# Kernel optimization log

Measured on AMD Instinct MI355X. Metric: run time of the kernel, lower is better.

The kernel has to match this reference:

```python
import jax, jax.numpy as jnp
import numpy as np

B, L, D, H, S, E, FF = 4, 2048, 1024, 16, 512, 8, 4096
DH = D // H  # head dim = 64
EPS = 1e-5


def setup_inputs() -> dict:
    key = jax.random.key(0)
    ks = jax.random.split(key, 12)
    std = 0.02
    return {
        "x": jax.random.normal(ks[0], (B, L, D), jnp.float32),
        "slot_query": jax.random.normal(ks[1], (H, S, DH), jnp.float32) * std,
        "slot_key": jax.random.normal(ks[2], (H, S, DH), jnp.float32) * std,
        "w_dispatch_k": jax.random.normal(ks[3], (D, D), jnp.float32) * std,
        "w_dispatch_v": jax.random.normal(ks[4], (D, D), jnp.float32) * std,
        "w_combine_q": jax.random.normal(ks[5], (D, D), jnp.float32) * std,
        "w_in": jax.random.normal(ks[6], (E, FF, D), jnp.float32) * std,
        "b_in": jnp.zeros((E, FF), jnp.float32),
        "w_out": jax.random.normal(ks[7], (E, D, FF), jnp.float32) * std,
        "b_out": jnp.zeros((E, D), jnp.float32),
        "pre_norm_w": jnp.ones((D,), jnp.float32),
        "pre_norm_b": jnp.zeros((D,), jnp.float32),
    }


def _layer_norm(x, w, b, eps=EPS):
    m = jnp.mean(x, axis=-1, keepdims=True)
    v = jnp.mean(jnp.square(x - m), axis=-1, keepdims=True)
    return (x - m) * jax.lax.rsqrt(v + eps) * w + b


def _sdpa(q, k, v):
    # q: (..., Q, d), k: (..., K, d), v: (..., K, d)
    scale = 1.0 / np.sqrt(q.shape[-1])
    scores = jnp.einsum("...qd,...kd->...qk", q, k) * scale
    p = jax.nn.softmax(scores, axis=-1)
    return jnp.einsum("...qk,...kd->...qd", p, v)


def _split_heads(t):  # (B, N, D) -> (B, H, N, DH)
    b, n, _ = t.shape
    return t.reshape(b, n, H, DH).transpose(0, 2, 1, 3)


def _merge_heads(t):  # (B, H, N, DH) -> (B, N, D)
    b, h, n, d = t.shape
    return t.transpose(0, 2, 1, 3).reshape(b, n, h * d)


def reference(x, slot_query, slot_key, w_dispatch_k, w_dispatch_v, w_combine_q,
              w_in, b_in, w_out, b_out, pre_norm_w, pre_norm_b):
    # pre-norm
    xn = _layer_norm(x, pre_norm_w, pre_norm_b)

    # ---- dispatch: slots attend to tokens ----
    k = _split_heads(xn @ w_dispatch_k.T)        # (B,H,L,DH)
    v = _split_heads(xn @ w_dispatch_v.T)        # (B,H,L,DH)
    y = _sdpa(slot_query[None], k, v)            # (B,H,S,DH)
    y = _merge_heads(y)                          # (B,S,D)

    # ---- experts: batched per-expert MLP with relu^2 activation ----
    y = y.reshape(B, E, S // E, D)
    h = jnp.einsum("besd,efd->besf", y, w_in) + b_in[None, :, None, :]
    h = jnp.square(jax.nn.relu(h))               # relu2
    eo = jnp.einsum("besf,edf->besd", h, w_out) + b_out[None, :, None, :]
    eo = eo.reshape(B, S, D)

    # ---- combine: tokens attend to slots ----
    q = _split_heads(xn @ w_combine_q.T)         # (B,H,L,DH)
    vc = _split_heads(eo)                        # (B,H,S,DH)
    o = _sdpa(q, slot_key[None], vc)             # (B,H,L,DH)
    return _merge_heads(o)                       # (B,L,D)
```

## Files before the change

### kernel.cpp

```cpp
#include <hip/hip_runtime.h>
#include <hip/hip_bf16.h>

#define B_  4
#define L_  2048
#define D_  1024
#define H_  16
#define S_  512
#define E_  8
#define FF_ 4096
#define DH_ 64

typedef _Float16 half8 __attribute__((ext_vector_type(8)));
typedef _Float16 half4v __attribute__((ext_vector_type(4)));
typedef float floatx4 __attribute__((ext_vector_type(4)));
typedef unsigned short u16;

__device__ inline u16 f2h(float v) {
  _Float16 x = (_Float16)v;
  return __builtin_bit_cast(u16, x);
}

__device__ inline void gload_lds16(const void* g, void* l) {
  __builtin_amdgcn_global_load_lds(
      (const __attribute__((address_space(1))) void*)g,
      (__attribute__((address_space(3))) void*)l, 16, 0, 0);
}

__device__ inline int swz(int row, int colh) {
  return row * 64 + (colh ^ ((row & 7) << 3));
}
__device__ inline int swz1(int row, int colh) {
  return row * 64 + ((colh & ~7) ^ ((row & 7) << 3)) + (colh & 7);
}

__global__ __launch_bounds__(256) void ln_f16(const float* __restrict__ x,
    const float* __restrict__ w, const float* __restrict__ bb,
    u16* __restrict__ xn) {
  int row = blockIdx.x;
  int tid = threadIdx.x;
  float4 v = ((const float4*)(x + (long)row * D_))[tid];
  float s = v.x + v.y + v.z + v.w;
  __shared__ float red[4];
  #pragma unroll
  for (int off = 32; off > 0; off >>= 1) s += __shfl_down(s, off);
  int wid = tid >> 6, lane = tid & 63;
  if (lane == 0) red[wid] = s;
  __syncthreads();
  float mean = (red[0] + red[1] + red[2] + red[3]) * (1.0f / D_);
  __syncthreads();
  float dx = v.x - mean, dy = v.y - mean, dz = v.z - mean, dw = v.w - mean;
  float s2 = dx*dx + dy*dy + dz*dz + dw*dw;
  #pragma unroll
  for (int off = 32; off > 0; off >>= 1) s2 += __shfl_down(s2, off);
  if (lane == 0) red[wid] = s2;
  __syncthreads();
  float var = (red[0] + red[1] + red[2] + red[3]) * (1.0f / D_);
  float rstd = rsqrtf(var + 1e-5f);
  float4 wv = ((const float4*)w)[tid];
  float4 bv = ((const float4*)bb)[tid];
  half4v o = { (_Float16)(dx * rstd * wv.x + bv.x),
               (_Float16)(dy * rstd * wv.y + bv.y),
               (_Float16)(dz * rstd * wv.z + bv.z),
               (_Float16)(dw * rstd * wv.w + bv.w) };
  *(half4v*)&xn[(long)row * D_ + tid * 4] = o;
}

__global__ __launch_bounds__(256) void wcvt(const float* __restrict__ w0,
    const float* __restrict__ w1, const float* __restrict__ w2,
    const float* __restrict__ sq, const float* __restrict__ skq,
    u16* __restrict__ dst) {
  long i = ((long)blockIdx.x * 256 + threadIdx.x) * 8;
  const float* src; long off; float sc = 1.0f;
  if (i < 3145728) {
    int wsel = (int)(i >> 20);
    src = (wsel == 0) ? w0 : (wsel == 1) ? w1 : w2;
    off = i & 1048575;
  } else if (i < 3670016) {
    src = sq; off = i - 3145728; sc = 0.125f;
  } else {
    src = skq; off = i - 3670016;
  }
  float4 a = *(const float4*)(src + off);
  float4 b = *(const float4*)(src + off + 4);
  half8 h = { (_Float16)(a.x*sc), (_Float16)(a.y*sc), (_Float16)(a.z*sc), (_Float16)(a.w*sc),
              (_Float16)(b.x*sc), (_Float16)(b.y*sc), (_Float16)(b.z*sc), (_Float16)(b.w*sc) };
  *(half8*)(dst + i) = h;
}

__global__ __launch_bounds__(256) void proj_f16(
    const u16* __restrict__ A, const u16* __restrict__ Wc,
    u16* __restrict__ kh, u16* __restrict__ vT, u16* __restrict__ qh) {
  const int wsel = blockIdx.x >> 3;
  const int n0 = (blockIdx.x & 7) * 128, m0 = blockIdx.y * 128;
  const u16* Bh = Wc + (long)wsel * 1048576;
  const int tid = threadIdx.x, l = tid & 63, w = tid >> 6;
  const int wr = w >> 1, wc = w & 1;
  __shared__ __align__(16) u16 As[2][128 * 32];
  __shared__ __align__(16) u16 Bs[2][128 * 32];
  floatx4 acc[4][4] = {};

  const int ck = (l & 3) ^ ((l >> 3) & 3);
  const long gaA0 = (long)(m0 + w * 32 + (l >> 2)) * D_ + ck * 8;
  const long gaA1 = gaA0 + 16 * D_;
  const long gaB0 = (long)(n0 + w * 32 + (l >> 2)) * D_ + ck * 8;
  const long gaB1 = gaB0 + 16 * D_;

  #define PSTAGE(buf, kt)                                          \
    do {                                                           \
      gload_lds16(A + gaA0 + (kt), &As[buf][(w * 32) * 32]);       \
      gload_lds16(A + gaA1 + (kt), &As[buf][(w * 32 + 16) * 32]);  \
      gload_lds16(Bh + gaB0 + (kt), &Bs[buf][(w * 32) * 32]);      \
      gload_lds16(Bh + gaB1 + (kt), &Bs[buf][(w * 32 + 16) * 32]); \
    } while (0)

  PSTAGE(0, 0);
  __syncthreads();

  int cur = 0;
  const int q = l >> 4;
  for (int t = 0; t < 32; ++t) {
    if (t < 31) PSTAGE(cur ^ 1, (t + 1) * 32);
    half8 af[4], bfr[4];
    #pragma unroll
    for (int fr = 0; fr < 4; ++fr) {
      int row = wr * 64 + fr * 16 + (l & 15);
      af[fr] = *(const half8*)&As[cur][row * 32 + ((q ^ ((row >> 1) & 3)) << 3)];
    }
    #pragma unroll
    for (int fc = 0; fc < 4; ++fc) {
      int rr = wc * 64 + fc * 16 + (l & 15);
      bfr[fc] = *(const half8*)&Bs[cur][rr * 32 + ((q ^ ((rr >> 1) & 3)) << 3)];
    }
    #pragma unroll
    for (int fr = 0; fr < 4; ++fr)
      #pragma unroll
      for (int fc = 0; fc < 4; ++fc)
        acc[fr][fc] = __builtin_amdgcn_mfma_f32_16x16x32_f16(af[fr], bfr[fc], acc[fr][fc], 0, 0, 0);
    __syncthreads();
    cur ^= 1;
  }
  #undef PSTAGE

  if (wsel == 1) {
    #pragma unroll
    for (int fr = 0; fr < 4; ++fr)
      #pragma unroll
      for (int fc = 0; fc < 4; ++fc) {
        int row = m0 + wr * 64 + fr * 16 + (l >> 4) * 4;
        int col = n0 + wc * 64 + fc * 16 + (l & 15);
        half4v o = { (_Float16)acc[fr][fc][0], (_Float16)acc[fr][fc][1],
                     (_Float16)acc[fr][fc][2], (_Float16)acc[fr][fc][3] };
        long idx = ((long)(row >> 11) * 1024 + col) * 2048 + (row & 2047);
        *(half4v*)&vT[idx] = o;
      }
  } else {
    u16* C = (wsel == 0) ? kh : qh;
    const float sc = (wsel == 2) ? 0.125f : 1.0f;
    #pragma unroll
    for (int fr = 0; fr < 4; ++fr)
      #pragma unroll
      for (int fc = 0; fc < 4; ++fc)
        #pragma unroll
        for (int r = 0; r < 4; ++r) {
          int row = m0 + wr * 64 + fr * 16 + (l >> 4) * 4 + r;
          int col = n0 + wc * 64 + fc * 16 + (l & 15);
          C[(long)row * D_ + col] = f2h(acc[fr][fc][r] * sc);
        }
  }
}

template<int MODE>
__global__ __launch_bounds__(512) void expert_gemm(
    const u16* __restrict__ A, const float* __restrict__ Bw,
    const float* __restrict__ bias, u16* __restrict__ Ch,
    float* __restrict__ Cp) {
  constexpr int LDA = (MODE == 1) ? D_ : FF_;
  constexpr int LDB = (MODE == 1) ? D_ : FF_;
  const int e = blockIdx.z;
  const int n0 = blockIdx.x * 64;
  const int kc0 = (MODE == 2) ? blockIdx.y * 1024 : 0;
  const int tid = threadIdx.x, l = tid & 63, w = tid >> 6;
  const int wm = w >> 1, wn = w & 1;
  const int lr = l & 15, q = l >> 4;

  __shared__ __align__(16) u16  As[2][256 * 32];
  __shared__ __align__(16) float Bs[2][64 * 32];

  long asrc[2];
  #pragma unroll
  for (int i = 0; i < 2; ++i) {
    int ar = w * 32 + i * 16 + (l >> 2);
    long grow = (MODE == 1) ? ((long)(ar >> 6) * 512 + e * 64 + (ar & 63))
                            : (((long)(ar >> 6) * 8 + e) * 64 + (ar & 63));
    int ck = (l & 3) ^ (ar & 3);
    asrc[i] = grow * (long)LDA + kc0 + ck * 8;
  }
  const float* Bp = Bw + (long)e * (D_ * FF_);
  int brow = w * 8 + (l >> 3);
  int bck = (l & 7) ^ (brow & 7);
  long bsrc = (long)(n0 + brow) * LDB + kc0 + bck * 4;

  floatx4 acc[4][2] = {};

  #define STAGE(buf, kt)                                                 \
    do {                                                                 \
      gload_lds16(A + asrc[0] + (kt), &As[buf][(w * 32) * 32]);          \
      gload_lds16(A + asrc[1] + (kt), &As[buf][(w * 32 + 16) * 32]);     \
      gload_lds16(Bp + bsrc + (kt), &Bs[buf][(w * 8) * 32]);             \
    } while (0)

  STAGE(0, 0);
  __syncthreads();

  int cur = 0;
  for (int t = 0; t < 32; ++t) {
    if (t < 31) STAGE(cur ^ 1, (t + 1) * 32);
    half8 af[4];
    #pragma unroll
    for (int fr = 0; fr < 4; ++fr) {
      int row = wm * 64 + fr * 16 + lr;
      af[fr] = *(const half8*)&As[cur][row * 32 + ((q ^ (row & 3)) << 3)];
    }
    half8 bf[2];
    #pragma unroll
    for (int fc = 0; fc < 2; ++fc) {
      int rn = wn * 32 + fc * 16 + lr;
      float4 x0 = *(const float4*)&Bs[cur][rn * 32 + (((2 * q) ^ (rn & 7)) << 2)];
      float4 x1 = *(const float4*)&Bs[cur][rn * 32 + (((2 * q + 1) ^ (rn & 7)) << 2)];
      bf[fc] = (half8){ (_Float16)x0.x, (_Float16)x0.y, (_Float16)x0.z, (_Float16)x0.w,
                        (_Float16)x1.x, (_Float16)x1.y, (_Float16)x1.z, (_Float16)x1.w };
    }
    #pragma unroll
    for (int fr = 0; fr < 4; ++fr)
      #pragma unroll
      for (int fc = 0; fc < 2; ++fc)
        acc[fr][fc] = __builtin_amdgcn_mfma_f32_16x16x32_f16(af[fr], bf[fc], acc[fr][fc], 0, 0, 0);
    __syncthreads();
    cur ^= 1;
  }
  #undef STAGE

  #pragma unroll
  for (int fr = 0; fr < 4; ++fr)
    #pragma unroll
    for (int fc = 0; fc < 2; ++fc)
      #pragma unroll
      for (int r = 0; r < 4; ++r) {
        int ar = wm * 64 + fr * 16 + q * 4 + r;
        int col = n0 + wn * 32 + fc * 16 + lr;
        float val = acc[fr][fc][r];
        if constexpr (MODE == 1) {
          val += bias[e * FF_ + col];
          val = fmaxf(val, 0.f);
          val *= val;
          Ch[(((long)(ar >> 6) * 8 + e) * 64 + (ar & 63)) * FF_ + col] = f2h(val);
        } else {
          Cp[(((long)blockIdx.y * 8 + e) * 256 + ar) * 1024 + col] = val;
        }
      }
}

__global__ __launch_bounds__(256) void eo_reduce(const float* __restrict__ pb,
    const float* __restrict__ b_out, u16* __restrict__ eoT) {
  long j4 = (long)blockIdx.x * 256 + threadIdx.x;
  long j = j4 * 4;
  float4 s = ((const float4*)pb)[j4];
  #pragma unroll
  for (int c = 1; c < 4; ++c) {
    float4 t = ((const float4*)(pb + (long)c * 2097152))[j4];
    s.x += t.x; s.y += t.y; s.z += t.z; s.w += t.w;
  }
  int e = (int)(j >> 18);
  int rem = (int)(j & 262143);
  int row = rem >> 10, col = rem & 1023;
  float4 bv = *(const float4*)(b_out + e * 1024 + col);
  s.x += bv.x; s.y += bv.y; s.z += bv.z; s.w += bv.w;
  int b = row >> 6;
  int slot = e * 64 + (row & 63);
  float sv[4] = { s.x, s.y, s.z, s.w };
  #pragma unroll
  for (int i = 0; i < 4; ++i) {
    long idx = ((long)b * 1024 + col + i) * 512 + slot;
    eoT[idx] = f2h(sv[i]);
  }
}

template<bool OF32>
__global__ __launch_bounds__(256) void flash_f16(
    const u16* __restrict__ Qg, long qB, long qH, long qR,
    const u16* __restrict__ Kg, long kB, long kH, long kR,
    const u16* __restrict__ VTg, long vB, long vH, long vR,
    void* __restrict__ Og, long oB, long oH, long oR,
    float* __restrict__ pd, float* __restrict__ pacc,
    int Nq, int Nk, int nC) {
  __shared__ __align__(16) u16 Ks[64 * 64];
  __shared__ __align__(16) u16 Vt[64 * 64];
  const int tid = threadIdx.x, l = tid & 63, w = tid >> 6;
  const int g = l >> 4, lq = l & 15;
  const int bh = blockIdx.z, b = bh >> 4, hd = bh & 15;
  const int q0 = blockIdx.x * 64 + w * 16;
  const int chunk = Nk / nC, k0 = blockIdx.y * chunk;

  half8 qf[2];
  #pragma unroll
  for (int ks = 0; ks < 2; ++ks)
    qf[ks] = *(const half8*)(Qg + b * qB + hd * qH +
                             (long)(q0 + lq) * qR + ks * 32 + g * 8);

  const int srow = l >> 3;
  const int scol = ((l & 7) ^ srow) * 8;
  const long kbase = b * kB + hd * kH;
  const long vbase = b * vB + hd * vH;

  float lrun = 0.f;
  floatx4 o[4] = {};

  for (int t = 0; t < chunk; t += 64) {
    #pragma unroll
    for (int i = 0; i < 2; ++i) {
      int u = i * 4 + w;
      gload_lds16(Kg + kbase + (long)(k0 + t + u * 8 + srow) * kR + scol,
                  &Ks[u * 8 * 64]);
      gload_lds16(VTg + vbase + (long)(u * 8 + srow) * vR + k0 + t + scol,
                  &Vt[u * 8 * 64]);
    }
    __syncthreads();

    floatx4 s[4];
    #pragma unroll
    for (int j = 0; j < 4; ++j) s[j] = (floatx4){0.f, 0.f, 0.f, 0.f};
    #pragma unroll
    for (int ks = 0; ks < 2; ++ks)
      #pragma unroll
      for (int j = 0; j < 4; ++j) {
        half8 kf = *(const half8*)&Ks[swz(j * 16 + lq, ks * 32 + g * 8)];
        s[j] = __builtin_amdgcn_mfma_f32_16x16x32_f16(kf, qf[ks], s[j], 0, 0, 0);
      }

    half4v pa[4];
    float rs = 0.f;
    #pragma unroll
    for (int j = 0; j < 4; ++j)
      #pragma unroll
      for (int r = 0; r < 4; ++r) {
        float p = __expf(s[j][r]);
        rs += p;
        pa[j][r] = (_Float16)p;
      }
    lrun += rs;

    #pragma unroll
    for (int j = 0; j < 4; ++j)
      #pragma unroll
      for (int n = 0; n < 4; ++n) {
        half4v vf = *(const half4v*)&Vt[swz1(n * 16 + lq, j * 16 + g * 4)];
        o[n] = __builtin_amdgcn_mfma_f32_16x16x16f16(pa[j], vf, o[n], 0, 0, 0);
      }
    __syncthreads();
  }

  lrun += __shfl_xor(lrun, 16);
  lrun += __shfl_xor(lrun, 32);

  if (nC == 1) {
    float inv = 1.0f / lrun;
    float invr[4];
    #pragma unroll
    for (int r = 0; r < 4; ++r) invr[r] = __shfl(inv, g * 4 + r);
    #pragma unroll
    for (int n = 0; n < 4; ++n)
      #pragma unroll
      for (int r = 0; r < 4; ++r) {
        int row = q0 + g * 4 + r;
        int dh = n * 16 + lq;
        float val = o[n][r] * invr[r];
        long off = b * oB + hd * oH + (long)row * oR + dh;
        if (OF32) ((float*)Og)[off] = val;
        else      ((u16*)Og)[off] = f2h(val);
      }
  } else {
    if (l < 16) pd[((long)bh * Nq + q0 + l) * nC + blockIdx.y] = lrun;
    #pragma unroll
    for (int r = 0; r < 4; ++r) {
      int row = q0 + g * 4 + r;
      long idx = ((long)bh * Nq + row) * nC + blockIdx.y;
      #pragma unroll
      for (int n = 0; n < 4; ++n)
        pacc[idx * 64 + n * 16 + lq] = o[n][r];
    }
  }
}

__global__ __launch_bounds__(256) void finalize_f16(
    const float* __restrict__ pd, const float* __restrict__ pacc,
    u16* __restrict__ outp, int nC, int Nq, long oB, long oH, long oR) {
  int tid = threadIdx.x;
  int row = blockIdx.x * 4 + (tid >> 6);
  int lane = tid & 63;
  long base = (long)row * nC;
  float Dn = 0.f, a = 0.f;
  for (int c = 0; c < nC; ++c) {
    Dn += pd[base + c];
    a += pacc[(base + c) * 64 + lane];
  }
  int bh = row / Nq, qrow = row - bh * Nq;
  int b = bh >> 4, h = bh & 15;
  outp[(long)b * oB + (long)h * oH + (long)qrow * oR + lane] = f2h(a / Dn);
}

extern "C" void kernel_launch(void* const* d_in, const int* in_sizes, int n_in,
                              void* d_out, int out_size, void* d_ws, size_t ws_size,
                              hipStream_t stream) {
  const float* x     = (const float*)d_in[0];
  const float* sq    = (const float*)d_in[1];
  const float* skq   = (const float*)d_in[2];
  const float* wk    = (const float*)d_in[3];
  const float* wv    = (const float*)d_in[4];
  const float* wq    = (const float*)d_in[5];
  const float* w_in  = (const float*)d_in[6];
  const float* b_in  = (const float*)d_in[7];
  const float* w_out = (const float*)d_in[8];
  const float* b_out = (const float*)d_in[9];
  const float* pnw   = (const float*)d_in[10];
  const float* pnb   = (const float*)d_in[11];
  float* out = (float*)d_out;

  u16* ws   = (u16*)d_ws;
  u16* xnh  = ws;
  u16* kh   = xnh + 8388608;
  u16* vTh  = kh  + 8388608;
  u16* qh   = vTh + 8388608;
  u16* yh   = qh  + 8388608;
  u16* hh   = yh  + 2097152;
  u16* eoTh = hh  + 8388608;
  u16* wch  = eoTh + 2097152;
  u16* sqh  = wch + 3145728;
  u16* skh  = wch + 3670016;
  float* pbuf = (float*)(wch + 4194304);
  float* pdb  = pbuf + 8388608;
  float* pacc = pbuf;

  ln_f16<<<8192, 256, 0, stream>>>(x, pnw, pnb, xnh);
  wcvt<<<2048, 256, 0, stream>>>(wk, wv, wq, sq, skq, wch);

  proj_f16<<<dim3(24, 64, 1), 256, 0, stream>>>(xnh, wch, kh, vTh, qh);

  flash_f16<false><<<dim3(8, 2, 64), 256, 0, stream>>>(
      sqh, 0L, (long)(S_ * DH_), (long)DH_,
      kh, (long)(L_ * D_), (long)DH_, (long)D_,
      vTh, (long)(L_ * D_), (long)(DH_ * L_), (long)L_,
      nullptr, 0L, 0L, 0L,
      pdb, pacc, S_, L_, 2);
  finalize_f16<<<8192, 256, 0, stream>>>(pdb, pacc, yh, 2, S_,
      (long)(S_ * D_), (long)DH_, (long)D_);

  expert_gemm<1><<<dim3(64, 1, 8), 512, 0, stream>>>(yh, w_in, b_in, hh, nullptr);
  expert_gemm<2><<<dim3(16, 4, 8), 512, 0, stream>>>(hh, w_out, nullptr, nullptr, pbuf);
  eo_reduce<<<2048, 256, 0, stream>>>(pbuf, b_out, eoTh);

  flash_f16<true><<<dim3(32, 1, 64), 256, 0, stream>>>(
      qh, (long)(L_ * D_), (long)DH_, (long)D_,
      skh, 0L, (long)(S_ * DH_), (long)DH_,
      eoTh, (long)(S_ * D_), (long)(DH_ * S_), (long)S_,
      out, (long)(L_ * D_), (long)DH_, (long)D_,
      nullptr, nullptr, L_, S_, 1);
}
```

Measured before the change: 318.5 us.

## Triple-buffer LDS staging in projection and expert GEMMs with one barrier per step

Converts the double-buffered global-to-LDS pipelines in proj_f16 and expert_gemm to three-stage ring buffers that prefetch two K-tiles ahead. Each iteration waits for its tile with explicit s_waitcnt vmcnt counts and one s_barrier, replacing the two __syncthreads per iteration. The goal is to hide more global load latency and cut barrier stalls. In exchange, shared memory grows by 50%, which may lower occupancy. Correctness now depends on the hand-set vmcnt counts matching the number of loads issued per stage.

Result: no change. 316.8 us (-0.5%).

```diff
diff --git a/kernel.cpp b/kernel.cpp
--- a/kernel.cpp
+++ b/kernel.cpp
@@ -95,8 +95,8 @@
   const u16* Bh = Wc + (long)wsel * 1048576;
   const int tid = threadIdx.x, l = tid & 63, w = tid >> 6;
   const int wr = w >> 1, wc = w & 1;
-  __shared__ __align__(16) u16 As[2][128 * 32];
-  __shared__ __align__(16) u16 Bs[2][128 * 32];
+  __shared__ __align__(16) u16 As[3][128 * 32];
+  __shared__ __align__(16) u16 Bs[3][128 * 32];
   floatx4 acc[4][4] = {};
 
   const int ck = (l & 3) ^ ((l >> 3) & 3);
@@ -114,30 +114,34 @@
     } while (0)
 
   PSTAGE(0, 0);
-  __syncthreads();
-
-  int cur = 0;
+  PSTAGE(1, 32);
+
+  int c0 = 0, c1 = 1, c2 = 2;
   const int q = l >> 4;
   for (int t = 0; t < 32; ++t) {
-    if (t < 31) PSTAGE(cur ^ 1, (t + 1) * 32);
+    if (t < 31) asm volatile("s_waitcnt vmcnt(4)" ::: "memory");
+    else        asm volatile("s_waitcnt vmcnt(0)" ::: "memory");
+    __builtin_amdgcn_s_barrier();
+    if (t + 2 < 32) PSTAGE(c2, (t + 2) * 32);
+
     half8 af[4], bfr[4];
     #pragma unroll
     for (int fr = 0; fr < 4; ++fr) {
       int row = wr * 64 + fr * 16 + (l & 15);
-      af[fr] = *(const half8*)&As[cur][row * 32 + ((q ^ ((row >> 1) & 3)) << 3)];
+      af[fr] = *(const half8*)&As[c0][row * 32 + ((q ^ ((row >> 1) & 3)) << 3)];
     }
     #pragma unroll
     for (int fc = 0; fc < 4; ++fc) {
       int rr = wc * 64 + fc * 16 + (l & 15);
-      bfr[fc] = *(const half8*)&Bs[cur][rr * 32 + ((q ^ ((rr >> 1) & 3)) << 3)];
+      bfr[fc] = *(const half8*)&Bs[c0][rr * 32 + ((q ^ ((rr >> 1) & 3)) << 3)];
     }
     #pragma unroll
     for (int fr = 0; fr < 4; ++fr)
       #pragma unroll
       for (int fc = 0; fc < 4; ++fc)
         acc[fr][fc] = __builtin_amdgcn_mfma_f32_16x16x32_f16(af[fr], bfr[fc], acc[fr][fc], 0, 0, 0);
-    __syncthreads();
-    cur ^= 1;
+
+    int tmp = c0; c0 = c1; c1 = c2; c2 = tmp;
   }
   #undef PSTAGE
 
@@ -183,8 +187,8 @@
   const int wm = w >> 1, wn = w & 1;
   const int lr = l & 15, q = l >> 4;
 
-  __shared__ __align__(16) u16  As[2][256 * 32];
-  __shared__ __align__(16) float Bs[2][64 * 32];
+  __shared__ __align__(16) u16  As[3][256 * 32];
+  __shared__ __align__(16) float Bs[3][64 * 32];
 
   long asrc[2];
   #pragma unroll
@@ -210,23 +214,27 @@
     } while (0)
 
   STAGE(0, 0);
-  __syncthreads();
-
-  int cur = 0;
+  STAGE(1, 32);
+
+  int c0 = 0, c1 = 1, c2 = 2;
   for (int t = 0; t < 32; ++t) {
-    if (t < 31) STAGE(cur ^ 1, (t + 1) * 32);
+    if (t < 31) asm volatile("s_waitcnt vmcnt(3)" ::: "memory");
+    else        asm volatile("s_waitcnt vmcnt(0)" ::: "memory");
+    __builtin_amdgcn_s_barrier();
+    if (t + 2 < 32) STAGE(c2, (t + 2) * 32);
+
     half8 af[4];
     #pragma unroll
     for (int fr = 0; fr < 4; ++fr) {
       int row = wm * 64 + fr * 16 + lr;
-      af[fr] = *(const half8*)&As[cur][row * 32 + ((q ^ (row & 3)) << 3)];
+      af[fr] = *(const half8*)&As[c0][row * 32 + ((q ^ (row & 3)) << 3)];
     }
     half8 bf[2];
     #pragma unroll
     for (int fc = 0; fc < 2; ++fc) {
       int rn = wn * 32 + fc * 16 + lr;
-      float4 x0 = *(const float4*)&Bs[cur][rn * 32 + (((2 * q) ^ (rn & 7)) << 2)];
-      float4 x1 = *(const float4*)&Bs[cur][rn * 32 + (((2 * q + 1) ^ (rn & 7)) << 2)];
+      float4 x0 = *(const float4*)&Bs[c0][rn * 32 + (((2 * q) ^ (rn & 7)) << 2)];
+      float4 x1 = *(const float4*)&Bs[c0][rn * 32 + (((2 * q + 1) ^ (rn & 7)) << 2)];
       bf[fc] = (half8){ (_Float16)x0.x, (_Float16)x0.y, (_Float16)x0.z, (_Float16)x0.w,
                         (_Float16)x1.x, (_Float16)x1.y, (_Float16)x1.z, (_Float16)x1.w };
     }
@@ -235,8 +243,8 @@
       #pragma unroll
       for (int fc = 0; fc < 2; ++fc)
         acc[fr][fc] = __builtin_amdgcn_mfma_f32_16x16x32_f16(af[fr], bf[fc], acc[fr][fc], 0, 0, 0);
-    __syncthreads();
-    cur ^= 1;
+
+    int tmp = c0; c0 = c1; c1 = c2; c2 = tmp;
   }
   #undef STAGE
 
```
